# Performance work log

Hardware: AMD Instinct MI355X
Metric: run time of the kernel (lower is better)

The kernel has to match this reference:

```python
import jax, jax.numpy as jnp
import numpy as np

N, M = 1024, 32
FN, FE = 64, 32
AGG_N, AGG_E = 128, 64
OUT_N, OUT_E = 64, 32


def _build_indices(n, m):
    nip, eip = [], []
    k = 0
    for i in range(1, n):
        j0 = max(0, i - m)
        nip += list(range(j0, i))
        eip += list(range(k, k + i - j0))
        k += i - j0
    n1 = np.array(nip, np.int32)
    eT = np.array(eip, np.int32)
    n2 = np.concatenate([np.full(min(i, m), i, np.int32) for i in range(1, n)])
    # padded previous-node window indices (0 = zero pad slot)
    prev_nodes = np.zeros(n * m, np.int32)
    k = 0
    for i in range(n):
        t = min(i, m)
        prev_nodes[(i + 1) * m - t:(i + 1) * m] = np.arange(k, k + t) + 1
        k += t
    n_e = k
    norm_node = np.full(n, 1.0 / m, np.float32)
    for i in range(1, m):
        norm_node[i] = 1.0 / i
    prev_edges = np.zeros(n_e * m, np.int32)
    k = 0
    e = 0
    for i in range(n):
        j0 = max(0, i - m)
        for j in range(j0, i):
            if j > j0:
                prev_edges[(e + 1) * m - (j - j0):(e + 1) * m] = np.arange(k, k + j - j0) + 1
            e += 1
        k += i - j0
    norm_edge = np.ones(n_e, np.float32)
    k = 0
    for i in range(1, n):
        t = min(i, m)
        for j in range(t):
            if j > 0:
                norm_edge[k] = 1.0 / j
            k += 1
    return n1, eT, n2, prev_nodes, norm_node, prev_edges, norm_edge, n_e

N1, ET, N2, PREV_N, NORM_N, PREV_E, NORM_E, NE = _build_indices(N, M)
N1 = jnp.asarray(N1); ET = jnp.asarray(ET); N2 = jnp.asarray(N2)
PREV_N = jnp.asarray(PREV_N); PREV_E = jnp.asarray(PREV_E)
NORM_N = jnp.asarray(NORM_N); NORM_E = jnp.asarray(NORM_E)


def setup_inputs() -> dict:
    key = jax.random.key(0)
    ks = jax.random.split(key, 20)
    s = 0.02
    inp = {
        'input_nodes': jax.random.normal(ks[0], (2, N, FN), jnp.float32),
        'input_edges': jax.random.normal(ks[1], (2, NE, FE), jnp.float32),
        # node-branch MLPs (exclude_last=False)
        'Wan1': jax.random.normal(ks[2], (2 * FN + FE, 2 * AGG_N)) * s,
        'ban1': jnp.zeros((2 * AGG_N,)),
        'Wan2': jax.random.normal(ks[3], (2 * AGG_N, AGG_N)) * s,
        'ban2': jnp.zeros((AGG_N,)),
        'Wln1': jax.random.normal(ks[4], (AGG_N + FN, AGG_N + FN)) * s,
        'bln1': jnp.zeros((AGG_N + FN,)),
        'Wln2': jax.random.normal(ks[5], (AGG_N + FN, OUT_N)) * s,
        'bln2': jnp.zeros((OUT_N,)),
        # edge-branch MLPs
        'Wae1': jax.random.normal(ks[6], (FN + FE, 2 * AGG_E)) * s,
        'bae1': jnp.zeros((2 * AGG_E,)),
        'Wae2': jax.random.normal(ks[7], (2 * AGG_E, AGG_E)) * s,
        'bae2': jnp.zeros((AGG_E,)),
        'Wle1': jax.random.normal(ks[8], (AGG_E + FE, AGG_E + FE)) * s,
        'ble1': jnp.zeros((AGG_E + FE,)),
        'Wle2': jax.random.normal(ks[9], (AGG_E + FE, OUT_E)) * s,
        'ble2': jnp.zeros((OUT_E,)),
    }
    return inp


def _mlp2(x, W1, b1, W2, b2):
    return jax.nn.relu(jax.nn.relu(x @ W1 + b1) @ W2 + b2)


def reference(input_nodes, input_edges, Wan1, ban1, Wan2, ban2, Wln1, bln1, Wln2, bln2,
              Wae1, bae1, Wae2, bae2, Wle1, ble1, Wle2, ble2):
    B = input_nodes.shape[0]
    # gather node-edge pairs [B, NE, FN+FE] and node-edge-node triples [B, NE, 2FN+FE]
    pairs = jnp.concatenate([input_nodes[:, N1], input_edges[:, ET]], axis=-1)
    triples = jnp.concatenate([input_nodes[:, N1], input_edges[:, ET], input_nodes[:, N2]], axis=-1)
    # node branch (exclude_last=False -> triples)
    hn = _mlp2(triples, Wan1, ban1, Wan2, ban2)                     # [B, NE, AGG_N]
    hn = jnp.concatenate([jnp.zeros((B, 1, AGG_N), hn.dtype), hn], axis=1)
    pn = hn[:, PREV_N].reshape(B, N, M, AGG_N).sum(axis=2)          # padded window sum
    pn = pn * NORM_N[None, :, None]
    nodes_in = jnp.concatenate([pn, input_nodes], axis=-1)
    out_nodes = _mlp2(nodes_in, Wln1, bln1, Wln2, bln2)             # activation_nodes = relu
    # edge branch (pairs)
    he = _mlp2(pairs, Wae1, bae1, Wae2, bae2)                       # [B, NE, AGG_E]
    he = jnp.concatenate([jnp.zeros((B, 1, AGG_E), he.dtype), he], axis=1)
    pe = he[:, PREV_E].reshape(B, NE, M, AGG_E).sum(axis=2)
    pe = pe * NORM_E[None, :, None]
    edges_in = jnp.concatenate([pe, input_edges], axis=-1)
    out_edges = _mlp2(edges_in, Wle1, ble1, Wle2, ble2)             # activation_edges = relu
    return out_nodes, out_edges
```

## Files before the change

kernel.cpp:

```cpp
#include <hip/hip_runtime.h>
#include <cstdint>

#define NN    1024
#define MM    32
#define NEDGE 32240
#define MROWS 64480
#define PX    168
#define PSTN  264

typedef unsigned short ushort_t;

typedef __bf16 bf16x8 __attribute__((ext_vector_type(8)));
typedef float  floatx4 __attribute__((ext_vector_type(4)));

__device__ __forceinline__ float b2f(ushort_t u) {
    union { unsigned int i; float f; } v; v.i = ((unsigned int)u) << 16; return v.f;
}
__device__ __forceinline__ ushort_t f2b(float f) {
    unsigned int u = __builtin_bit_cast(unsigned int, f);
    u = (u + 0x7FFFu + ((u >> 16) & 1u)) >> 16;
    return (ushort_t)u;
}
__device__ __forceinline__ int edge_base(int i) {
    return (i <= MM) ? ((i * (i - 1)) >> 1) : (496 + (i - MM) * MM);
}
__device__ __forceinline__ void edge_ij(int e, int& i, int& j) {
    if (e < 496) {
        i = (int)((1.0f + sqrtf(8.0f * (float)e + 1.0f)) * 0.5f);
        while (((i * (i - 1)) >> 1) > e) --i;
        while (((i * (i + 1)) >> 1) <= e) ++i;
        j = e - ((i * (i - 1)) >> 1);
    } else {
        int q = e - 496;
        i = MM + (q >> 5);
        j = i - MM + (q & 31);
    }
}

__global__ __launch_bounds__(256) void k_pack(
        const float* an1, const float* an2, const float* ae1, const float* ae2,
        const float* le1, const float* le2, const float* ln1, const float* ln2,
        const float* nodes, const float* edges,
        ushort_t* pan1, ushort_t* pan2, ushort_t* pae1, ushort_t* pae2,
        ushort_t* ple1, ushort_t* ple2, ushort_t* pln1, ushort_t* pln2,
        ushort_t* nodesb, ushort_t* edgesb, int2* ijt) {
    __shared__ float tile[32][33];
    const int bid = blockIdx.x;
    const int tid = threadIdx.x;
    if (bid < 152) {
        const float* s; ushort_t* d; int K, N, t;
        if (bid < 40)       { s = an1; d = pan1; K = 160; N = 256; t = bid;       }
        else if (bid < 72)  { s = an2; d = pan2; K = 256; N = 128; t = bid - 40;  }
        else if (bid < 84)  { s = ae1; d = pae1; K = 96;  N = 128; t = bid - 72;  }
        else if (bid < 92)  { s = ae2; d = pae2; K = 128; N = 64;  t = bid - 84;  }
        else if (bid < 101) { s = le1; d = ple1; K = 96;  N = 96;  t = bid - 92;  }
        else if (bid < 104) { s = le2; d = ple2; K = 96;  N = 32;  t = bid - 101; }
        else if (bid < 140) { s = ln1; d = pln1; K = 192; N = 192; t = bid - 104; }
        else                { s = ln2; d = pln2; K = 192; N = 64;  t = bid - 140; }
        int ntn = N >> 5;
        int tk = t / ntn, tn = t - tk * ntn;
        int k0 = tk * 32, n0 = tn * 32;
        int tx = tid & 31, ty = tid >> 5;
#pragma unroll
        for (int m = 0; m < 4; ++m)
            tile[ty + m * 8][tx] = s[(size_t)(k0 + ty + m * 8) * N + n0 + tx];
        __syncthreads();
#pragma unroll
        for (int m = 0; m < 4; ++m)
            d[(size_t)(n0 + ty + m * 8) * K + k0 + tx] = f2b(tile[tx][ty + m * 8]);
    } else if (bid < 280) {
        int i4 = (bid - 152) * 256 + tid;
        float4 v = ((const float4*)nodes)[i4];
        uint2 o;
        o.x = (unsigned)f2b(v.x) | ((unsigned)f2b(v.y) << 16);
        o.y = (unsigned)f2b(v.z) | ((unsigned)f2b(v.w) << 16);
        ((uint2*)nodesb)[i4] = o;
    } else if (bid < 2296) {
        int i4 = (bid - 280) * 256 + tid;
        if (i4 < 515840) {
            float4 v = ((const float4*)edges)[i4];
            uint2 o;
            o.x = (unsigned)f2b(v.x) | ((unsigned)f2b(v.y) << 16);
            o.y = (unsigned)f2b(v.z) | ((unsigned)f2b(v.w) << 16);
            ((uint2*)edgesb)[i4] = o;
        }
    } else {
        int e = (bid - 2296) * 256 + tid;
        if (e < NEDGE) { int i, j; edge_ij(e, i, j); ijt[e] = make_int2(i, j); }
    }
}

__global__ __launch_bounds__(512, 2) void k_agg(
        const ushort_t* __restrict__ nodesb, const ushort_t* __restrict__ edgesb,
        const int2* __restrict__ ijt,
        const ushort_t* __restrict__ pan1, const float* __restrict__ ban1,
        const ushort_t* __restrict__ pan2, const float* __restrict__ ban2,
        ushort_t* __restrict__ hn) {
    __shared__ alignas(16) ushort_t X[32 * PX];
    __shared__ alignas(16) ushort_t H[32 * PSTN];
    const int tid = threadIdx.x;
    const int w = tid >> 6, l = tid & 63, lrow = l & 15, lq = l >> 4;
    const int mt = blockIdx.x;
    floatx4 zero = {0.f, 0.f, 0.f, 0.f};

    bf16x8 B0[5], B1[5];
#pragma unroll
    for (int kt = 0; kt < 5; ++kt) {
        B0[kt] = *(const bf16x8*)(pan1 + (size_t)(16 * w + lrow) * 160 + kt * 32 + lq * 8);
        B1[kt] = *(const bf16x8*)(pan1 + (size_t)(16 * (w + 8) + lrow) * 160 + kt * 32 + lq * 8);
    }
    float c0 = ban1[16 * w + lrow];
    float c1 = ban1[16 * (w + 8) + lrow];

#pragma unroll
    for (int k = 0; k < 4; ++k) {
        int rr = w * 4 + k;
        int r = mt * 32 + rr;
        int off = (r >= NEDGE) ? 1 : 0;
        int2 ij = ijt[r - off * NEDGE];
        int bN = off * NN;
        unsigned* xr = (unsigned*)(X + rr * PX);
        const unsigned* nj = (const unsigned*)(nodesb + (size_t)(bN + ij.y) * 64);
        const unsigned* ni = (const unsigned*)(nodesb + (size_t)(bN + ij.x) * 64);
        const unsigned* eb = (const unsigned*)(edgesb + (size_t)r * 32);
        if (l < 32) { xr[l] = nj[l]; xr[48 + l] = ni[l]; }
        else        xr[l] = eb[l - 32];
    }
    __syncthreads();

#pragma unroll
    for (int s = 0; s < 2; ++s) {
        bf16x8 A[5];
#pragma unroll
        for (int kt = 0; kt < 5; ++kt)
            A[kt] = *(const bf16x8*)&X[(s * 16 + lrow) * PX + kt * 32 + lq * 8];
        floatx4 a0 = zero, a1 = zero;
#pragma unroll
        for (int kt = 0; kt < 5; ++kt) {
            a0 = __builtin_amdgcn_mfma_f32_16x16x32_bf16(A[kt], B0[kt], a0, 0, 0, 0);
            a1 = __builtin_amdgcn_mfma_f32_16x16x32_bf16(A[kt], B1[kt], a1, 0, 0, 0);
        }
#pragma unroll
        for (int r_ = 0; r_ < 4; ++r_) {
            int row = (s * 16 + lq * 4 + r_) * PSTN;
            H[row + 16 * w + lrow]       = f2b(fmaxf(a0[r_] + c0, 0.f));
            H[row + 128 + 16 * w + lrow] = f2b(fmaxf(a1[r_] + c1, 0.f));
        }
    }
    __syncthreads();

    {
        bf16x8 D[8];
#pragma unroll
        for (int kt = 0; kt < 8; ++kt)
            D[kt] = *(const bf16x8*)(pan2 + (size_t)(16 * w + lrow) * 256 + kt * 32 + lq * 8);
        float d0 = ban2[16 * w + lrow];
#pragma unroll
        for (int s = 0; s < 2; ++s) {
            floatx4 a0 = zero;
#pragma unroll
            for (int kt = 0; kt < 8; ++kt) {
                bf16x8 a = *(const bf16x8*)&H[(s * 16 + lrow) * PSTN + kt * 32 + lq * 8];
                a0 = __builtin_amdgcn_mfma_f32_16x16x32_bf16(a, D[kt], a0, 0, 0, 0);
            }
#pragma unroll
            for (int r_ = 0; r_ < 4; ++r_)
                X[(s * 16 + lq * 4 + r_) * 136 + 16 * w + lrow] = f2b(fmaxf(a0[r_] + d0, 0.f));
        }
    }
    __syncthreads();

    {
        int row = tid >> 4, c = tid & 15;
        ((uint4*)(hn + (size_t)(mt * 32 + row) * 128))[c] = *(const uint4*)&X[row * 136 + c * 8];
    }
}

#define PXE 104
#define PH1 136
#define PHE 72
__global__ __launch_bounds__(256) void k_edge(
        const ushort_t* __restrict__ nodesb, const ushort_t* __restrict__ edgesb,
        const ushort_t* __restrict__ pae1, const float* __restrict__ bae1,
        const ushort_t* __restrict__ pae2, const float* __restrict__ bae2,
        const ushort_t* __restrict__ ple1, const float* __restrict__ ble1,
        const ushort_t* __restrict__ ple2, const float* __restrict__ ble2,
        float* __restrict__ out_edges) {
    __shared__ alignas(16) ushort_t X[32 * PXE];
    __shared__ alignas(16) ushort_t H1[32 * PH1];
    __shared__ alignas(16) ushort_t HE[32 * PHE];
    __shared__ alignas(16) ushort_t LB[32 * PXE];
    const int tid = threadIdx.x;
    const int w = tid >> 6, l = tid & 63, lrow = l & 15, lq = l >> 4;
    const int b = blockIdx.x >> 10, i = blockIdx.x & 1023;
    const int t = min(i, MM);
    if (t == 0) return;
    const int j0 = i - t;
    const int base = b * NEDGE + edge_base(i);
    floatx4 zero = {0.f, 0.f, 0.f, 0.f};

    bf16x8 B0[3], B1[3];
#pragma unroll
    for (int kt = 0; kt < 3; ++kt) {
        B0[kt] = *(const bf16x8*)(pae1 + (size_t)(16 * w + lrow) * 96 + kt * 32 + lq * 8);
        B1[kt] = *(const bf16x8*)(pae1 + (size_t)(16 * (w + 4) + lrow) * 96 + kt * 32 + lq * 8);
    }
    const float c0 = bae1[16 * w + lrow];
    const float c1 = bae1[16 * (w + 4) + lrow];

    for (int u = tid; u < 32 * 48; u += 256) {
        int row = u / 48, c = u - row * 48;
        unsigned v;
        if (c < 32) v = ((const unsigned*)nodesb)[(size_t)(b * NN + j0 + row) * 32 + c];
        else        v = ((const unsigned*)edgesb)[(size_t)(base + row) * 16 + (c - 32)];
        ((unsigned*)X)[row * (PXE / 2) + c] = v;
    }
    __syncthreads();

#pragma unroll
    for (int s = 0; s < 2; ++s) {
        bf16x8 A[3];
#pragma unroll
        for (int kt = 0; kt < 3; ++kt)
            A[kt] = *(const bf16x8*)&X[(s * 16 + lrow) * PXE + kt * 32 + lq * 8];
        floatx4 a0 = zero, a1 = zero;
#pragma unroll
        for (int kt = 0; kt < 3; ++kt) {
            a0 = __builtin_amdgcn_mfma_f32_16x16x32_bf16(A[kt], B0[kt], a0, 0, 0, 0);
            a1 = __builtin_amdgcn_mfma_f32_16x16x32_bf16(A[kt], B1[kt], a1, 0, 0, 0);
        }
#pragma unroll
        for (int r_ = 0; r_ < 4; ++r_) {
            int row = (s * 16 + lq * 4 + r_) * PH1;
            H1[row + 16 * w + lrow]      = f2b(fmaxf(a0[r_] + c0, 0.f));
            H1[row + 64 + 16 * w + lrow] = f2b(fmaxf(a1[r_] + c1, 0.f));
        }
    }
    __syncthreads();

    {
        bf16x8 E[4];
#pragma unroll
        for (int kt = 0; kt < 4; ++kt)
            E[kt] = *(const bf16x8*)(pae2 + (size_t)(16 * w + lrow) * 128 + kt * 32 + lq * 8);
        float d2 = bae2[16 * w + lrow];
#pragma unroll
        for (int s = 0; s < 2; ++s) {
            floatx4 a2 = zero;
#pragma unroll
            for (int kt = 0; kt < 4; ++kt) {
                bf16x8 a = *(const bf16x8*)&H1[(s * 16 + lrow) * PH1 + kt * 32 + lq * 8];
                a2 = __builtin_amdgcn_mfma_f32_16x16x32_bf16(a, E[kt], a2, 0, 0, 0);
            }
#pragma unroll
            for (int r_ = 0; r_ < 4; ++r_)
                HE[(s * 16 + lq * 4 + r_) * PHE + 16 * w + lrow] = f2b(fmaxf(a2[r_] + d2, 0.f));
        }
    }
    if (l < 16) {
        float run = 0.f;
        for (int p = 0; p < t; ++p) {
            X[p * PXE + 16 * w + l] = f2b((p == 0) ? 0.f : run / (float)p);
            run += b2f(HE[p * PHE + 16 * w + l]);
        }
    }
    __syncthreads();

    {
        bf16x8 F0[3], F1[3];
        const bool two = (w < 2);
#pragma unroll
        for (int kt = 0; kt < 3; ++kt) {
            F0[kt] = *(const bf16x8*)(ple1 + (size_t)(16 * w + lrow) * 96 + kt * 32 + lq * 8);
            if (two)
                F1[kt] = *(const bf16x8*)(ple1 + (size_t)(16 * (w + 4) + lrow) * 96 + kt * 32 + lq * 8);
        }
        float v0 = ble1[16 * w + lrow];
        float v1 = two ? ble1[16 * (w + 4) + lrow] : 0.f;
#pragma unroll
        for (int s = 0; s < 2; ++s) {
            bf16x8 A[3];
#pragma unroll
            for (int kt = 0; kt < 3; ++kt)
                A[kt] = *(const bf16x8*)&X[(s * 16 + lrow) * PXE + kt * 32 + lq * 8];
            floatx4 a0 = zero, a1 = zero;
#pragma unroll
            for (int kt = 0; kt < 3; ++kt) {
                a0 = __builtin_amdgcn_mfma_f32_16x16x32_bf16(A[kt], F0[kt], a0, 0, 0, 0);
                if (two)
                    a1 = __builtin_amdgcn_mfma_f32_16x16x32_bf16(A[kt], F1[kt], a1, 0, 0, 0);
            }
#pragma unroll
            for (int r_ = 0; r_ < 4; ++r_) {
                int row = (s * 16 + lq * 4 + r_) * PXE;
                LB[row + 16 * w + lrow] = f2b(fmaxf(a0[r_] + v0, 0.f));
                if (two)
                    LB[row + 64 + 16 * w + lrow] = f2b(fmaxf(a1[r_] + v1, 0.f));
            }
        }
    }
    __syncthreads();

    {
        int ct = w & 1, s = w >> 1;
        int c0o = 16 * ct;
        bf16x8 F2[3];
#pragma unroll
        for (int kt = 0; kt < 3; ++kt)
            F2[kt] = *(const bf16x8*)(ple2 + (size_t)(c0o + lrow) * 96 + kt * 32 + lq * 8);
        float v2 = ble2[c0o + lrow];
        floatx4 a2 = zero;
#pragma unroll
        for (int kt = 0; kt < 3; ++kt) {
            bf16x8 a = *(const bf16x8*)&LB[(s * 16 + lrow) * PXE + kt * 32 + lq * 8];
            a2 = __builtin_amdgcn_mfma_f32_16x16x32_bf16(a, F2[kt], a2, 0, 0, 0);
        }
#pragma unroll
        for (int r_ = 0; r_ < 4; ++r_) {
            int grow = s * 16 + lq * 4 + r_;
            if (grow < t)
                out_edges[(size_t)(base + grow) * 32 + c0o + lrow] = fmaxf(a2[r_] + v2, 0.f);
        }
    }
}

__global__ __launch_bounds__(256) void k_mid(
        const ushort_t* __restrict__ hn, ushort_t* __restrict__ pn) {
    const int tid = threadIdx.x;
    int ri = blockIdx.x;
    int b = ri >> 10, i = ri & 1023;
    int t = min(i, MM);
    int base = b * NEDGE + edge_base(i);
    int c = tid & 63, g = tid >> 6;
    float s0 = 0.f, s1 = 0.f;
    for (int p = g; p < t; p += 4) {
        unsigned u = ((const unsigned*)(hn + (size_t)(base + p) * 128))[c];
        s0 += b2f((ushort_t)(u & 0xffff));
        s1 += b2f((ushort_t)(u >> 16));
    }
    __shared__ float red[4][128];
    red[g][c * 2] = s0; red[g][c * 2 + 1] = s1;
    __syncthreads();
    if (tid < 64) {
        float inv = 1.0f / (float)max(t, 1);
        float a0 = (red[0][tid * 2] + red[1][tid * 2] + red[2][tid * 2] + red[3][tid * 2]) * inv;
        float a1 = (red[0][tid * 2 + 1] + red[1][tid * 2 + 1] + red[2][tid * 2 + 1] + red[3][tid * 2 + 1]) * inv;
        ((unsigned*)(pn + (size_t)ri * 128))[tid] = (unsigned)f2b(a0) | ((unsigned)f2b(a1) << 16);
    }
}

__global__ __launch_bounds__(192) void k_final(
        const ushort_t* __restrict__ pn, const ushort_t* __restrict__ nodesb,
        const ushort_t* __restrict__ pln1, const float* __restrict__ bln1,
        const ushort_t* __restrict__ pln2, const float* __restrict__ bln2,
        float* __restrict__ out_nodes) {
    __shared__ alignas(16) ushort_t LA[32 * 200];
    __shared__ alignas(16) ushort_t LB[32 * 200];
    const int tid = threadIdx.x;
    const int w = tid >> 6, l = tid & 63, lrow = l & 15, lq = l >> 4;
    floatx4 zero = {0.f, 0.f, 0.f, 0.f};

    int tile = blockIdx.x;
    for (int u = tid; u < 768; u += 192) {
        int row = u / 24, c = u - row * 24;
        int r = tile * 32 + row;
        const uint4* src = (c < 16) ? ((const uint4*)(pn + (size_t)r * 128) + c)
                                    : ((const uint4*)(nodesb + (size_t)r * 64) + (c - 16));
        *(uint4*)&LA[row * 200 + c * 8] = *src;
    }
    bf16x8 f1[6][4]; float v1[4];
#pragma unroll
    for (int kt = 0; kt < 6; ++kt)
#pragma unroll
        for (int nt = 0; nt < 4; ++nt)
            f1[kt][nt] = *(const bf16x8*)(pln1 + (size_t)(w * 64 + nt * 16 + lrow) * 192 + kt * 32 + lq * 8);
#pragma unroll
    for (int nt = 0; nt < 4; ++nt) v1[nt] = bln1[w * 64 + nt * 16 + lrow];
    __syncthreads();

    floatx4 acc[2][4];
#pragma unroll
    for (int s = 0; s < 2; ++s)
#pragma unroll
        for (int nt = 0; nt < 4; ++nt) acc[s][nt] = zero;
#pragma unroll
    for (int s = 0; s < 2; ++s)
#pragma unroll
        for (int kt = 0; kt < 6; ++kt) {
            bf16x8 a = *(const bf16x8*)&LA[(s * 16 + lrow) * 200 + kt * 32 + lq * 8];
#pragma unroll
            for (int nt = 0; nt < 4; ++nt)
                acc[s][nt] = __builtin_amdgcn_mfma_f32_16x16x32_bf16(a, f1[kt][nt], acc[s][nt], 0, 0, 0);
        }
#pragma unroll
    for (int s = 0; s < 2; ++s)
#pragma unroll
        for (int nt = 0; nt < 4; ++nt) {
            int col = w * 64 + nt * 16 + lrow;
#pragma unroll
            for (int r_ = 0; r_ < 4; ++r_)
                LB[(s * 16 + lq * 4 + r_) * 200 + col] = f2b(fmaxf(acc[s][nt][r_] + v1[nt], 0.f));
        }
    bf16x8 f2[6][2]; float v2[2] = {0.f, 0.f};
    if (w < 2) {
#pragma unroll
        for (int kt = 0; kt < 6; ++kt)
#pragma unroll
            for (int nt = 0; nt < 2; ++nt)
                f2[kt][nt] = *(const bf16x8*)(pln2 + (size_t)(w * 32 + nt * 16 + lrow) * 192 + kt * 32 + lq * 8);
#pragma unroll
        for (int nt = 0; nt < 2; ++nt) v2[nt] = bln2[w * 32 + nt * 16 + lrow];
    }
    __syncthreads();
    if (w < 2) {
        floatx4 a2[2][2];
#pragma unroll
        for (int s = 0; s < 2; ++s) { a2[s][0] = zero; a2[s][1] = zero; }
#pragma unroll
        for (int s = 0; s < 2; ++s)
#pragma unroll
            for (int kt = 0; kt < 6; ++kt) {
                bf16x8 a = *(const bf16x8*)&LB[(s * 16 + lrow) * 200 + kt * 32 + lq * 8];
#pragma unroll
                for (int nt = 0; nt < 2; ++nt)
                    a2[s][nt] = __builtin_amdgcn_mfma_f32_16x16x32_bf16(a, f2[kt][nt], a2[s][nt], 0, 0, 0);
            }
#pragma unroll
        for (int s = 0; s < 2; ++s)
#pragma unroll
            for (int nt = 0; nt < 2; ++nt) {
                int col = w * 32 + nt * 16 + lrow;
#pragma unroll
                for (int r_ = 0; r_ < 4; ++r_)
                    out_nodes[(size_t)(tile * 32 + s * 16 + lq * 4 + r_) * 64 + col] =
                        fmaxf(a2[s][nt][r_] + v2[nt], 0.f);
            }
    }
}

extern "C" void kernel_launch(void* const* d_in, const int* in_sizes, int n_in,
                              void* d_out, int out_size, void* d_ws, size_t ws_size,
                              hipStream_t stream) {
    const float* nodes = (const float*)d_in[0];
    const float* edges = (const float*)d_in[1];
    const float* Wan1 = (const float*)d_in[2];  const float* ban1 = (const float*)d_in[3];
    const float* Wan2 = (const float*)d_in[4];  const float* ban2 = (const float*)d_in[5];
    const float* Wln1 = (const float*)d_in[6];  const float* bln1 = (const float*)d_in[7];
    const float* Wln2 = (const float*)d_in[8];  const float* bln2 = (const float*)d_in[9];
    const float* Wae1 = (const float*)d_in[10]; const float* bae1 = (const float*)d_in[11];
    const float* Wae2 = (const float*)d_in[12]; const float* bae2 = (const float*)d_in[13];
    const float* Wle1 = (const float*)d_in[14]; const float* ble1 = (const float*)d_in[15];
    const float* Wle2 = (const float*)d_in[16]; const float* ble2 = (const float*)d_in[17];

    char* ws = (char*)d_ws;
    size_t o = 0;
    auto alloc = [&](size_t bytes) -> void* {
        void* r = ws + o;
        o += (bytes + 255) & ~(size_t)255;
        return r;
    };
    ushort_t* hn     = (ushort_t*)alloc((size_t)MROWS * 128 * 2);
    ushort_t* pn     = (ushort_t*)alloc((size_t)2048 * 128 * 2);
    ushort_t* nodesb = (ushort_t*)alloc((size_t)2 * NN * 64 * 2);
    ushort_t* edgesb = (ushort_t*)alloc((size_t)MROWS * 32 * 2);
    int2*     ijt    = (int2*)alloc((size_t)NEDGE * 8);
    ushort_t* pan1 = (ushort_t*)alloc(160 * 256 * 2);
    ushort_t* pan2 = (ushort_t*)alloc(256 * 128 * 2);
    ushort_t* pae1 = (ushort_t*)alloc(96 * 128 * 2);
    ushort_t* pae2 = (ushort_t*)alloc(128 * 64 * 2);
    ushort_t* ple1 = (ushort_t*)alloc(96 * 96 * 2);
    ushort_t* ple2 = (ushort_t*)alloc(96 * 32 * 2);
    ushort_t* pln1 = (ushort_t*)alloc(192 * 192 * 2);
    ushort_t* pln2 = (ushort_t*)alloc(192 * 64 * 2);

    float* out_nodes = (float*)d_out;
    float* out_edges = (float*)d_out + 2 * NN * 64;

    k_pack<<<2422, 256, 0, stream>>>(Wan1, Wan2, Wae1, Wae2, Wle1, Wle2, Wln1, Wln2,
                                     nodes, edges,
                                     pan1, pan2, pae1, pae2, ple1, ple2, pln1, pln2,
                                     nodesb, edgesb, ijt);
    k_agg<<<2015, 512, 0, stream>>>(nodesb, edgesb, ijt,
                                    pan1, ban1, pan2, ban2, hn);
    k_edge<<<2048, 256, 0, stream>>>(nodesb, edgesb,
                                     pae1, bae1, pae2, bae2,
                                     ple1, ble1, ple2, ble2, out_edges);
    k_mid<<<2048, 256, 0, stream>>>(hn, pn);
    k_final<<<64, 192, 0, stream>>>(pn, nodesb, pln1, bln1, pln2, bln2, out_nodes);

    (void)in_sizes; (void)n_in; (void)out_size; (void)ws_size;
}
```

Measured before the change: 171.5 us.

## Fuse node aggregation MLP, window sum and edge branch into one kernel

Merges k_agg, k_mid and k_edge into a single k_main launch. Node-branch blocks now each process one destination node's window of up to 32 edges. They run the two-layer MLP and reduce the window sum in shared memory, so the hn intermediate is never written to or read back from global memory. Edge-branch blocks handle two rows per 512-thread block, and the ijt index table is dropped because the node window layout is computed directly. The cost is that padded rows are computed wastefully for small windows, and there are more launch-bounds (occupancy) constraints.

```diff
diff --git a/kernel.cpp b/kernel.cpp
--- a/kernel.cpp
+++ b/kernel.cpp
@@ -7,6 +7,9 @@
 #define MROWS 64480
 #define PX    168
 #define PSTN  264
+#define PXE   104
+#define PH1   136
+#define PHE   72
 
 typedef unsigned short ushort_t;
 
@@ -23,18 +26,6 @@
 }
 __device__ __forceinline__ int edge_base(int i) {
     return (i <= MM) ? ((i * (i - 1)) >> 1) : (496 + (i - MM) * MM);
-}
-__device__ __forceinline__ void edge_ij(int e, int& i, int& j) {
-    if (e < 496) {
-        i = (int)((1.0f + sqrtf(8.0f * (float)e + 1.0f)) * 0.5f);
-        while (((i * (i - 1)) >> 1) > e) --i;
-        while (((i * (i + 1)) >> 1) <= e) ++i;
-        j = e - ((i * (i - 1)) >> 1);
-    } else {
-        int q = e - 496;
-        i = MM + (q >> 5);
-        j = i - MM + (q & 31);
-    }
 }
 
 __global__ __launch_bounds__(256) void k_pack(
@@ -43,7 +34,7 @@
         const float* nodes, const float* edges,
         ushort_t* pan1, ushort_t* pan2, ushort_t* pae1, ushort_t* pae2,
         ushort_t* ple1, ushort_t* ple2, ushort_t* pln1, ushort_t* pln2,
-        ushort_t* nodesb, ushort_t* edgesb, int2* ijt) {
+        ushort_t* nodesb, ushort_t* edgesb) {
     __shared__ float tile[32][33];
     const int bid = blockIdx.x;
     const int tid = threadIdx.x;
@@ -75,7 +66,7 @@
         o.x = (unsigned)f2b(v.x) | ((unsigned)f2b(v.y) << 16);
         o.y = (unsigned)f2b(v.z) | ((unsigned)f2b(v.w) << 16);
         ((uint2*)nodesb)[i4] = o;
-    } else if (bid < 2296) {
+    } else {
         int i4 = (bid - 280) * 256 + tid;
         if (i4 < 515840) {
             float4 v = ((const float4*)edges)[i4];
@@ -84,268 +75,261 @@
             o.y = (unsigned)f2b(v.z) | ((unsigned)f2b(v.w) << 16);
             ((uint2*)edgesb)[i4] = o;
         }
-    } else {
-        int e = (bid - 2296) * 256 + tid;
-        if (e < NEDGE) { int i, j; edge_ij(e, i, j); ijt[e] = make_int2(i, j); }
     }
 }
 
-__global__ __launch_bounds__(512, 2) void k_agg(
+__global__ __launch_bounds__(512, 4) void k_main(
         const ushort_t* __restrict__ nodesb, const ushort_t* __restrict__ edgesb,
-        const int2* __restrict__ ijt,
         const ushort_t* __restrict__ pan1, const float* __restrict__ ban1,
         const ushort_t* __restrict__ pan2, const float* __restrict__ ban2,
-        ushort_t* __restrict__ hn) {
-    __shared__ alignas(16) ushort_t X[32 * PX];
-    __shared__ alignas(16) ushort_t H[32 * PSTN];
-    const int tid = threadIdx.x;
-    const int w = tid >> 6, l = tid & 63, lrow = l & 15, lq = l >> 4;
-    const int mt = blockIdx.x;
-    floatx4 zero = {0.f, 0.f, 0.f, 0.f};
-
-    bf16x8 B0[5], B1[5];
-#pragma unroll
-    for (int kt = 0; kt < 5; ++kt) {
-        B0[kt] = *(const bf16x8*)(pan1 + (size_t)(16 * w + lrow) * 160 + kt * 32 + lq * 8);
-        B1[kt] = *(const bf16x8*)(pan1 + (size_t)(16 * (w + 8) + lrow) * 160 + kt * 32 + lq * 8);
-    }
-    float c0 = ban1[16 * w + lrow];
-    float c1 = ban1[16 * (w + 8) + lrow];
-
-#pragma unroll
-    for (int k = 0; k < 4; ++k) {
-        int rr = w * 4 + k;
-        int r = mt * 32 + rr;
-        int off = (r >= NEDGE) ? 1 : 0;
-        int2 ij = ijt[r - off * NEDGE];
-        int bN = off * NN;
-        unsigned* xr = (unsigned*)(X + rr * PX);
-        const unsigned* nj = (const unsigned*)(nodesb + (size_t)(bN + ij.y) * 64);
-        const unsigned* ni = (const unsigned*)(nodesb + (size_t)(bN + ij.x) * 64);
-        const unsigned* eb = (const unsigned*)(edgesb + (size_t)r * 32);
-        if (l < 32) { xr[l] = nj[l]; xr[48 + l] = ni[l]; }
-        else        xr[l] = eb[l - 32];
-    }
-    __syncthreads();
-
-#pragma unroll
-    for (int s = 0; s < 2; ++s) {
-        bf16x8 A[5];
-#pragma unroll
-        for (int kt = 0; kt < 5; ++kt)
-            A[kt] = *(const bf16x8*)&X[(s * 16 + lrow) * PX + kt * 32 + lq * 8];
-        floatx4 a0 = zero, a1 = zero;
-#pragma unroll
-        for (int kt = 0; kt < 5; ++kt) {
-            a0 = __builtin_amdgcn_mfma_f32_16x16x32_bf16(A[kt], B0[kt], a0, 0, 0, 0);
-            a1 = __builtin_amdgcn_mfma_f32_16x16x32_bf16(A[kt], B1[kt], a1, 0, 0, 0);
-        }
-#pragma unroll
-        for (int r_ = 0; r_ < 4; ++r_) {
-            int row = (s * 16 + lq * 4 + r_) * PSTN;
-            H[row + 16 * w + lrow]       = f2b(fmaxf(a0[r_] + c0, 0.f));
-            H[row + 128 + 16 * w + lrow] = f2b(fmaxf(a1[r_] + c1, 0.f));
-        }
-    }
-    __syncthreads();
-
-    {
-        bf16x8 D[8];
-#pragma unroll
-        for (int kt = 0; kt < 8; ++kt)
-            D[kt] = *(const bf16x8*)(pan2 + (size_t)(16 * w + lrow) * 256 + kt * 32 + lq * 8);
-        float d0 = ban2[16 * w + lrow];
-#pragma unroll
-        for (int s = 0; s < 2; ++s) {
-            floatx4 a0 = zero;
-#pragma unroll
-            for (int kt = 0; kt < 8; ++kt) {
-                bf16x8 a = *(const bf16x8*)&H[(s * 16 + lrow) * PSTN + kt * 32 + lq * 8];
-                a0 = __builtin_amdgcn_mfma_f32_16x16x32_bf16(a, D[kt], a0, 0, 0, 0);
-            }
-#pragma unroll
-            for (int r_ = 0; r_ < 4; ++r_)
-                X[(s * 16 + lq * 4 + r_) * 136 + 16 * w + lrow] = f2b(fmaxf(a0[r_] + d0, 0.f));
-        }
-    }
-    __syncthreads();
-
-    {
-        int row = tid >> 4, c = tid & 15;
-        ((uint4*)(hn + (size_t)(mt * 32 + row) * 128))[c] = *(const uint4*)&X[row * 136 + c * 8];
-    }
-}
-
-#define PXE 104
-#define PH1 136
-#define PHE 72
-__global__ __launch_bounds__(256) void k_edge(
-        const ushort_t* __restrict__ nodesb, const ushort_t* __restrict__ edgesb,
         const ushort_t* __restrict__ pae1, const float* __restrict__ bae1,
         const ushort_t* __restrict__ pae2, const float* __restrict__ bae2,
         const ushort_t* __restrict__ ple1, const float* __restrict__ ble1,
         const ushort_t* __restrict__ ple2, const float* __restrict__ ble2,
-        float* __restrict__ out_edges) {
-    __shared__ alignas(16) ushort_t X[32 * PXE];
-    __shared__ alignas(16) ushort_t H1[32 * PH1];
-    __shared__ alignas(16) ushort_t HE[32 * PHE];
-    __shared__ alignas(16) ushort_t LB[32 * PXE];
+        ushort_t* __restrict__ pn, float* __restrict__ out_edges) {
+    __shared__ alignas(16) ushort_t SH[26624];
     const int tid = threadIdx.x;
     const int w = tid >> 6, l = tid & 63, lrow = l & 15, lq = l >> 4;
-    const int b = blockIdx.x >> 10, i = blockIdx.x & 1023;
-    const int t = min(i, MM);
-    if (t == 0) return;
-    const int j0 = i - t;
-    const int base = b * NEDGE + edge_base(i);
+    const int bid = blockIdx.x;
     floatx4 zero = {0.f, 0.f, 0.f, 0.f};
 
-    bf16x8 B0[3], B1[3];
-#pragma unroll
-    for (int kt = 0; kt < 3; ++kt) {
-        B0[kt] = *(const bf16x8*)(pae1 + (size_t)(16 * w + lrow) * 96 + kt * 32 + lq * 8);
-        B1[kt] = *(const bf16x8*)(pae1 + (size_t)(16 * (w + 4) + lrow) * 96 + kt * 32 + lq * 8);
-    }
-    const float c0 = bae1[16 * w + lrow];
-    const float c1 = bae1[16 * (w + 4) + lrow];
-
-    for (int u = tid; u < 32 * 48; u += 256) {
-        int row = u / 48, c = u - row * 48;
-        unsigned v;
-        if (c < 32) v = ((const unsigned*)nodesb)[(size_t)(b * NN + j0 + row) * 32 + c];
-        else        v = ((const unsigned*)edgesb)[(size_t)(base + row) * 16 + (c - 32)];
-        ((unsigned*)X)[row * (PXE / 2) + c] = v;
-    }
-    __syncthreads();
-
-#pragma unroll
-    for (int s = 0; s < 2; ++s) {
-        bf16x8 A[3];
-#pragma unroll
-        for (int kt = 0; kt < 3; ++kt)
-            A[kt] = *(const bf16x8*)&X[(s * 16 + lrow) * PXE + kt * 32 + lq * 8];
-        floatx4 a0 = zero, a1 = zero;
+    if (bid < 2048) {
+        const int b = bid >> 10, i = bid & 1023;
+        const int t = min(i, MM);
+        if (i == 0) {
+            if (tid < 64) ((unsigned*)(pn + (size_t)bid * 128))[tid] = 0u;
+            return;
+        }
+        const int j0 = i - t;
+        const int base = b * NEDGE + edge_base(i);
+        ushort_t* X = SH;
+        ushort_t* H = SH + 32 * PX;
+
+        bf16x8 B0[5], B1[5];
+#pragma unroll
+        for (int kt = 0; kt < 5; ++kt) {
+            B0[kt] = *(const bf16x8*)(pan1 + (size_t)(16 * w + lrow) * 160 + kt * 32 + lq * 8);
+            B1[kt] = *(const bf16x8*)(pan1 + (size_t)(16 * (w + 8) + lrow) * 160 + kt * 32 + lq * 8);
+        }
+        float c0 = ban1[16 * w + lrow];
+        float c1 = ban1[16 * (w + 8) + lrow];
+
+#pragma unroll
+        for (int k = 0; k < 4; ++k) {
+            int rr = w * 4 + k;
+            unsigned* xr = (unsigned*)(X + rr * PX);
+            const unsigned* nj = (const unsigned*)(nodesb + (size_t)(b * NN + j0 + rr) * 64);
+            const unsigned* ni = (const unsigned*)(nodesb + (size_t)(b * NN + i) * 64);
+            const unsigned* eb = (const unsigned*)(edgesb + (size_t)(base + rr) * 32);
+            if (l < 32) { xr[l] = nj[l]; xr[48 + l] = ni[l]; }
+            else        xr[l] = eb[l - 32];
+        }
+        __syncthreads();
+
+#pragma unroll
+        for (int s = 0; s < 2; ++s) {
+            bf16x8 A[5];
+#pragma unroll
+            for (int kt = 0; kt < 5; ++kt)
+                A[kt] = *(const bf16x8*)&X[(s * 16 + lrow) * PX + kt * 32 + lq * 8];
+            floatx4 a0 = zero, a1 = zero;
+#pragma unroll
+            for (int kt = 0; kt < 5; ++kt) {
+                a0 = __builtin_amdgcn_mfma_f32_16x16x32_bf16(A[kt], B0[kt], a0, 0, 0, 0);
+                a1 = __builtin_amdgcn_mfma_f32_16x16x32_bf16(A[kt], B1[kt], a1, 0, 0, 0);
+            }
+#pragma unroll
+            for (int r_ = 0; r_ < 4; ++r_) {
+                int row = (s * 16 + lq * 4 + r_) * PSTN;
+                H[row + 16 * w + lrow]       = f2b(fmaxf(a0[r_] + c0, 0.f));
+                H[row + 128 + 16 * w + lrow] = f2b(fmaxf(a1[r_] + c1, 0.f));
+            }
+        }
+        __syncthreads();
+
+        {
+            bf16x8 D[8];
+#pragma unroll
+            for (int kt = 0; kt < 8; ++kt)
+                D[kt] = *(const bf16x8*)(pan2 + (size_t)(16 * w + lrow) * 256 + kt * 32 + lq * 8);
+            float d0 = ban2[16 * w + lrow];
+#pragma unroll
+            for (int s = 0; s < 2; ++s) {
+                floatx4 a0 = zero;
+#pragma unroll
+                for (int kt = 0; kt < 8; ++kt) {
+                    bf16x8 a = *(const bf16x8*)&H[(s * 16 + lrow) * PSTN + kt * 32 + lq * 8];
+                    a0 = __builtin_amdgcn_mfma_f32_16x16x32_bf16(a, D[kt], a0, 0, 0, 0);
+                }
+#pragma unroll
+                for (int r_ = 0; r_ < 4; ++r_)
+                    X[(s * 16 + lq * 4 + r_) * 136 + 16 * w + lrow] = f2b(fmaxf(a0[r_] + d0, 0.f));
+            }
+        }
+        __syncthreads();
+
+        {
+            int c = tid & 63, g = tid >> 6;
+            float s0 = 0.f, s1 = 0.f;
+            for (int p = g; p < t; p += 8) {
+                unsigned u = ((const unsigned*)X)[p * 68 + c];
+                s0 += b2f((ushort_t)(u & 0xffff));
+                s1 += b2f((ushort_t)(u >> 16));
+            }
+            float* red = (float*)(SH + 32 * PX);
+            red[g * 128 + 2 * c]     = s0;
+            red[g * 128 + 2 * c + 1] = s1;
+            __syncthreads();
+            if (tid < 64) {
+                float inv = 1.0f / (float)t;
+                float a0 = 0.f, a1 = 0.f;
+#pragma unroll
+                for (int g2 = 0; g2 < 8; ++g2) {
+                    a0 += red[g2 * 128 + 2 * tid];
+                    a1 += red[g2 * 128 + 2 * tid + 1];
+                }
+                a0 *= inv; a1 *= inv;
+                ((unsigned*)(pn + (size_t)bid * 128))[tid] =
+                    (unsigned)f2b(a0) | ((unsigned)f2b(a1) << 16);
+            }
+        }
+    } else {
+        const int q = bid - 2048;
+        const int h = w >> 2, w4 = w & 3;
+        const int lt = tid & 255;
+        const int ri = 2 * q + h;
+        const int b = ri >> 10, i = ri & 1023;
+        const int t = min(i, MM);
+        const int j0 = i - t;
+        const int base = b * NEDGE + edge_base(i);
+        ushort_t* Xe = SH + h * 13312;
+        ushort_t* H1 = Xe + 3328;
+        ushort_t* HE = H1 + 4352;
+        ushort_t* LB = HE + 2304;
+
+        bf16x8 B0[3], B1[3];
 #pragma unroll
         for (int kt = 0; kt < 3; ++kt) {
-            a0 = __builtin_amdgcn_mfma_f32_16x16x32_bf16(A[kt], B0[kt], a0, 0, 0, 0);
-            a1 = __builtin_amdgcn_mfma_f32_16x16x32_bf16(A[kt], B1[kt], a1, 0, 0, 0);
-        }
-#pragma unroll
-        for (int r_ = 0; r_ < 4; ++r_) {
-            int row = (s * 16 + lq * 4 + r_) * PH1;
-            H1[row + 16 * w + lrow]      = f2b(fmaxf(a0[r_] + c0, 0.f));
-            H1[row + 64 + 16 * w + lrow] = f2b(fmaxf(a1[r_] + c1, 0.f));
-        }
-    }
-    __syncthreads();
-
-    {
-        bf16x8 E[4];
-#pragma unroll
-        for (int kt = 0; kt < 4; ++kt)
-            E[kt] = *(const bf16x8*)(pae2 + (size_t)(16 * w + lrow) * 128 + kt * 32 + lq * 8);
-        float d2 = bae2[16 * w + lrow];
-#pragma unroll
-        for (int s = 0; s < 2; ++s) {
-            floatx4 a2 = zero;
-#pragma unroll
-            for (int kt = 0; kt < 4; ++kt) {
-                bf16x8 a = *(const bf16x8*)&H1[(s * 16 + lrow) * PH1 + kt * 32 + lq * 8];
-                a2 = __builtin_amdgcn_mfma_f32_16x16x32_bf16(a, E[kt], a2, 0, 0, 0);
-            }
-#pragma unroll
-            for (int r_ = 0; r_ < 4; ++r_)
-                HE[(s * 16 + lq * 4 + r_) * PHE + 16 * w + lrow] = f2b(fmaxf(a2[r_] + d2, 0.f));
-        }
-    }
-    if (l < 16) {
-        float run = 0.f;
-        for (int p = 0; p < t; ++p) {
-            X[p * PXE + 16 * w + l] = f2b((p == 0) ? 0.f : run / (float)p);
-            run += b2f(HE[p * PHE + 16 * w + l]);
-        }
-    }
-    __syncthreads();
-
-    {
-        bf16x8 F0[3], F1[3];
-        const bool two = (w < 2);
-#pragma unroll
-        for (int kt = 0; kt < 3; ++kt) {
-            F0[kt] = *(const bf16x8*)(ple1 + (size_t)(16 * w + lrow) * 96 + kt * 32 + lq * 8);
-            if (two)
-                F1[kt] = *(const bf16x8*)(ple1 + (size_t)(16 * (w + 4) + lrow) * 96 + kt * 32 + lq * 8);
-        }
-        float v0 = ble1[16 * w + lrow];
-        float v1 = two ? ble1[16 * (w + 4) + lrow] : 0.f;
+            B0[kt] = *(const bf16x8*)(pae1 + (size_t)(16 * w4 + lrow) * 96 + kt * 32 + lq * 8);
+            B1[kt] = *(const bf16x8*)(pae1 + (size_t)(16 * (w4 + 4) + lrow) * 96 + kt * 32 + lq * 8);
+        }
+        const float c0 = bae1[16 * w4 + lrow];
+        const float c1 = bae1[16 * (w4 + 4) + lrow];
+
+        for (int u = lt; u < 32 * 48; u += 256) {
+            int row = u / 48, c = u - row * 48;
+            unsigned v;
+            if (c < 32) v = ((const unsigned*)nodesb)[(size_t)(b * NN + j0 + row) * 32 + c];
+            else        v = ((const unsigned*)edgesb)[(size_t)(base + row) * 16 + (c - 32)];
+            ((unsigned*)Xe)[row * (PXE / 2) + c] = v;
+        }
+        __syncthreads();
+
 #pragma unroll
         for (int s = 0; s < 2; ++s) {
             bf16x8 A[3];
 #pragma unroll
             for (int kt = 0; kt < 3; ++kt)
-                A[kt] = *(const bf16x8*)&X[(s * 16 + lrow) * PXE + kt * 32 + lq * 8];
+                A[kt] = *(const bf16x8*)&Xe[(s * 16 + lrow) * PXE + kt * 32 + lq * 8];
             floatx4 a0 = zero, a1 = zero;
 #pragma unroll
             for (int kt = 0; kt < 3; ++kt) {
-                a0 = __builtin_amdgcn_mfma_f32_16x16x32_bf16(A[kt], F0[kt], a0, 0, 0, 0);
+                a0 = __builtin_amdgcn_mfma_f32_16x16x32_bf16(A[kt], B0[kt], a0, 0, 0, 0);
+                a1 = __builtin_amdgcn_mfma_f32_16x16x32_bf16(A[kt], B1[kt], a1, 0, 0, 0);
+            }
+#pragma unroll
+            for (int r_ = 0; r_ < 4; ++r_) {
+                int row = (s * 16 + lq * 4 + r_) * PH1;
+                H1[row + 16 * w4 + lrow]      = f2b(fmaxf(a0[r_] + c0, 0.f));
+                H1[row + 64 + 16 * w4 + lrow] = f2b(fmaxf(a1[r_] + c1, 0.f));
+            }
+        }
+        __syncthreads();
+
+        {
+            bf16x8 E[4];
+#pragma unroll
+            for (int kt = 0; kt < 4; ++kt)
+                E[kt] = *(const bf16x8*)(pae2 + (size_t)(16 * w4 + lrow) * 128 + kt * 32 + lq * 8);
+            float d2 = bae2[16 * w4 + lrow];
+#pragma unroll
+            for (int s = 0; s < 2; ++s) {
+                floatx4 a2 = zero;
+#pragma unroll
+                for (int kt = 0; kt < 4; ++kt) {
+                    bf16x8 a = *(const bf16x8*)&H1[(s * 16 + lrow) * PH1 + kt * 32 + lq * 8];
+                    a2 = __builtin_amdgcn_mfma_f32_16x16x32_bf16(a, E[kt], a2, 0, 0, 0);
+                }
+#pragma unroll
+                for (int r_ = 0; r_ < 4; ++r_)
+                    HE[(s * 16 + lq * 4 + r_) * PHE + 16 * w4 + lrow] = f2b(fmaxf(a2[r_] + d2, 0.f));
+            }
+        }
+        if (l < 16) {
+            float run = 0.f;
+            for (int p = 0; p < t; ++p) {
+                Xe[p * PXE + 16 * w4 + l] = f2b((p == 0) ? 0.f : run / (float)p);
+                run += b2f(HE[p * PHE + 16 * w4 + l]);
+            }
+        }
+        __syncthreads();
+
+        {
+            bf16x8 F0[3], F1[3];
+            const bool two = (w4 < 2);
+#pragma unroll
+            for (int kt = 0; kt < 3; ++kt) {
+                F0[kt] = *(const bf16x8*)(ple1 + (size_t)(16 * w4 + lrow) * 96 + kt * 32 + lq * 8);
                 if (two)
-                    a1 = __builtin_amdgcn_mfma_f32_16x16x32_bf16(A[kt], F1[kt], a1, 0, 0, 0);
+                    F1[kt] = *(const bf16x8*)(ple1 + (size_t)(16 * (w4 + 4) + lrow) * 96 + kt * 32 + lq * 8);
+            }
+            float v0 = ble1[16 * w4 + lrow];
+            float v1 = two ? ble1[16 * (w4 + 4) + lrow] : 0.f;
+#pragma unroll
+            for (int s = 0; s < 2; ++s) {
+                bf16x8 A[3];
+#pragma unroll
+                for (int kt = 0; kt < 3; ++kt)
+                    A[kt] = *(const bf16x8*)&Xe[(s * 16 + lrow) * PXE + kt * 32 + lq * 8];
+                floatx4 a0 = zero, a1 = zero;
+#pragma unroll
+                for (int kt = 0; kt < 3; ++kt) {
+                    a0 = __builtin_amdgcn_mfma_f32_16x16x32_bf16(A[kt], F0[kt], a0, 0, 0, 0);
+                    if (two)
+                        a1 = __builtin_amdgcn_mfma_f32_16x16x32_bf16(A[kt], F1[kt], a1, 0, 0, 0);
+                }
+#pragma unroll
+                for (int r_ = 0; r_ < 4; ++r_) {
+                    int row = (s * 16 + lq * 4 + r_) * PXE;
+                    LB[row + 16 * w4 + lrow] = f2b(fmaxf(a0[r_] + v0, 0.f));
+                    if (two)
+                        LB[row + 64 + 16 * w4 + lrow] = f2b(fmaxf(a1[r_] + v1, 0.f));
+                }
+            }
+        }
+        __syncthreads();
+
+        {
+            int ct = w4 & 1, s = w4 >> 1;
+            int c0o = 16 * ct;
+            bf16x8 F2[3];
+#pragma unroll
+            for (int kt = 0; kt < 3; ++kt)
+                F2[kt] = *(const bf16x8*)(ple2 + (size_t)(c0o + lrow) * 96 + kt * 32 + lq * 8);
+            float v2 = ble2[c0o + lrow];
+            floatx4 a2 = zero;
+#pragma unroll
+            for (int kt = 0; kt < 3; ++kt) {
+                bf16x8 a = *(const bf16x8*)&LB[(s * 16 + lrow) * PXE + kt * 32 + lq * 8];
+                a2 = __builtin_amdgcn_mfma_f32_16x16x32_bf16(a, F2[kt], a2, 0, 0, 0);
             }
 #pragma unroll
             for (int r_ = 0; r_ < 4; ++r_) {
-                int row = (s * 16 + lq * 4 + r_) * PXE;
-                LB[row + 16 * w + lrow] = f2b(fmaxf(a0[r_] + v0, 0.f));
-                if (two)
-                    LB[row + 64 + 16 * w + lrow] = f2b(fmaxf(a1[r_] + v1, 0.f));
-            }
-        }
-    }
-    __syncthreads();
-
-    {
-        int ct = w & 1, s = w >> 1;
-        int c0o = 16 * ct;
-        bf16x8 F2[3];
-#pragma unroll
-        for (int kt = 0; kt < 3; ++kt)
-            F2[kt] = *(const bf16x8*)(ple2 + (size_t)(c0o + lrow) * 96 + kt * 32 + lq * 8);
-        float v2 = ble2[c0o + lrow];
-        floatx4 a2 = zero;
-#pragma unroll
-        for (int kt = 0; kt < 3; ++kt) {
-            bf16x8 a = *(const bf16x8*)&LB[(s * 16 + lrow) * PXE + kt * 32 + lq * 8];
-            a2 = __builtin_amdgcn_mfma_f32_16x16x32_bf16(a, F2[kt], a2, 0, 0, 0);
-        }
-#pragma unroll
-        for (int r_ = 0; r_ < 4; ++r_) {
-            int grow = s * 16 + lq * 4 + r_;
-            if (grow < t)
-                out_edges[(size_t)(base + grow) * 32 + c0o + lrow] = fmaxf(a2[r_] + v2, 0.f);
-        }
-    }
-}
-
-__global__ __launch_bounds__(256) void k_mid(
-        const ushort_t* __restrict__ hn, ushort_t* __restrict__ pn) {
-    const int tid = threadIdx.x;
-    int ri = blockIdx.x;
-    int b = ri >> 10, i = ri & 1023;
-    int t = min(i, MM);
-    int base = b * NEDGE + edge_base(i);
-    int c = tid & 63, g = tid >> 6;
-    float s0 = 0.f, s1 = 0.f;
-    for (int p = g; p < t; p += 4) {
-        unsigned u = ((const unsigned*)(hn + (size_t)(base + p) * 128))[c];
-        s0 += b2f((ushort_t)(u & 0xffff));
-        s1 += b2f((ushort_t)(u >> 16));
-    }
-    __shared__ float red[4][128];
-    red[g][c * 2] = s0; red[g][c * 2 + 1] = s1;
-    __syncthreads();
-    if (tid < 64) {
-        float inv = 1.0f / (float)max(t, 1);
-        float a0 = (red[0][tid * 2] + red[1][tid * 2] + red[2][tid * 2] + red[3][tid * 2]) * inv;
-        float a1 = (red[0][tid * 2 + 1] + red[1][tid * 2 + 1] + red[2][tid * 2 + 1] + red[3][tid * 2 + 1]) * inv;
-        ((unsigned*)(pn + (size_t)ri * 128))[tid] = (unsigned)f2b(a0) | ((unsigned)f2b(a1) << 16);
+                int grow = s * 16 + lq * 4 + r_;
+                if (grow < t)
+                    out_edges[(size_t)(base + grow) * 32 + c0o + lrow] = fmaxf(a2[r_] + v2, 0.f);
+            }
+        }
     }
 }
 
@@ -459,11 +443,9 @@
         o += (bytes + 255) & ~(size_t)255;
         return r;
     };
-    ushort_t* hn     = (ushort_t*)alloc((size_t)MROWS * 128 * 2);
     ushort_t* pn     = (ushort_t*)alloc((size_t)2048 * 128 * 2);
     ushort_t* nodesb = (ushort_t*)alloc((size_t)2 * NN * 64 * 2);
     ushort_t* edgesb = (ushort_t*)alloc((size_t)MROWS * 32 * 2);
-    int2*     ijt    = (int2*)alloc((size_t)NEDGE * 8);
     ushort_t* pan1 = (ushort_t*)alloc(160 * 256 * 2);
     ushort_t* pan2 = (ushort_t*)alloc(256 * 128 * 2);
     ushort_t* pae1 = (ushort_t*)alloc(96 * 128 * 2);
@@ -476,16 +458,15 @@
     float* out_nodes = (float*)d_out;
     float* out_edges = (float*)d_out + 2 * NN * 64;
 
-    k_pack<<<2422, 256, 0, stream>>>(Wan1, Wan2, Wae1, Wae2, Wle1, Wle2, Wln1, Wln2,
+    k_pack<<<2296, 256, 0, stream>>>(Wan1, Wan2, Wae1, Wae2, Wle1, Wle2, Wln1, Wln2,
                                      nodes, edges,
                                      pan1, pan2, pae1, pae2, ple1, ple2, pln1, pln2,
-                                     nodesb, edgesb, ijt);
-    k_agg<<<2015, 512, 0, stream>>>(nodesb, edgesb, ijt,
-                                    pan1, ban1, pan2, ban2, hn);
-    k_edge<<<2048, 256, 0, stream>>>(nodesb, edgesb,
+                                     nodesb, edgesb);
+    k_main<<<3072, 512, 0, stream>>>(nodesb, edgesb,
+                                     pan1, ban1, pan2, ban2,
                                      pae1, bae1, pae2, bae2,
-                                     ple1, ble1, ple2, ble2, out_edges);
-    k_mid<<<2048, 256, 0, stream>>>(hn, pn);
+                                     ple1, ble1, ple2, ble2,
+                                     pn, out_edges);
     k_final<<<64, 192, 0, stream>>>(pn, nodesb, pln1, bln1, pln2, bln2, out_nodes);
 
     (void)in_sizes; (void)n_in; (void)out_size; (void)ws_size;
```

New measurement: 158.5 us. 1.08x faster.
